# Performance work log

Measured on AMD Instinct MI355X. Metric: run time of the kernel, lower is better.

The kernel has to match this reference:

```python
import jax, jax.numpy as jnp
import numpy as np

N_NODES = 50000
N_EDGES = 800000
FEATURES = 64
HIDDEN = 128
OUT_DIM = 64
CUTOFF = 10.0
STEP = 0.1
N_MU = 100  # len(arange(0, 10, 0.1))


def setup_inputs() -> dict:
    key = jax.random.key(0)
    k_h, k_src, k_dst, k_norm, k_w1, k_w2 = jax.random.split(key, 6)
    h = jax.random.normal(k_h, (N_NODES, FEATURES), dtype=jnp.float32)
    src = jax.random.randint(k_src, (N_EDGES,), 0, N_NODES, dtype=jnp.int64)
    dst = jax.random.randint(k_dst, (N_EDGES,), 0, N_NODES, dtype=jnp.int64)
    edge_norm = jax.random.uniform(k_norm, (N_EDGES,), dtype=jnp.float32) * CUTOFF
    mu = jnp.arange(0.0, CUTOFF, STEP, dtype=jnp.float32)  # [100], learned param
    in_dim = 2 * FEATURES + N_MU
    # xavier_normal with gain split across 2 linear layers: layer_gain = 1.0
    s1 = float(np.sqrt(2.0 / (in_dim + HIDDEN)))
    s2 = float(np.sqrt(2.0 / (HIDDEN + OUT_DIM)))
    W1 = jax.random.normal(k_w1, (HIDDEN, in_dim), dtype=jnp.float32) * s1
    W2 = jax.random.normal(k_w2, (OUT_DIM, HIDDEN), dtype=jnp.float32) * s2
    return {"h": h, "src": src, "dst": dst, "edge_norm": edge_norm,
            "mu": mu, "W1": W1, "W2": W2}


def reference(h, src, dst, edge_norm, mu, W1, W2):
    # Gaussian RBF expansion of edge distances: [E, n_mu]
    d_emb = jnp.exp((-1.0 / STEP) * (mu[None, :] - edge_norm[:, None]) ** 2)
    # gather endpoint features and concat: [E, 2*features + n_mu]
    x = jnp.concatenate((h[src], h[dst], d_emb), axis=-1)
    # MLP: Linear(no bias) -> SiLU -> Linear(no bias)
    hdn = jax.nn.silu(x @ W1.T)
    return hdn @ W2.T
```

## Files before the change

kernel.cpp:

```cpp
#include <hip/hip_runtime.h>
#include <hip/hip_bf16.h>

#define FEAT     64
#define NMU      100
#define K1_REAL  228
#define K1_PAD   256
#define HID      128
#define ODIM     64
#define K2       128
#define MTILE    64
#define LDA1     264
#define LDH      132

typedef __bf16 bf16x8 __attribute__((ext_vector_type(8)));
typedef __bf16 bf16x4 __attribute__((ext_vector_type(4)));
typedef float  fx4    __attribute__((ext_vector_type(4)));

__global__ void pack_w(const float* __restrict__ W1, const float* __restrict__ W2,
                       __bf16* __restrict__ B1, __bf16* __restrict__ B2) {
    int i = blockIdx.x * 256 + threadIdx.x;
    if (i < 32768) {
        int j  = i & 7;
        int n  = (i >> 3) & 127;
        int qk = i >> 10;
        int k  = (qk >> 2) * 32 + (qk & 3) * 8 + j;
        float v = (k < K1_REAL) ? W1[n * K1_REAL + k] : 0.0f;
        B1[i] = (__bf16)v;
    } else {
        int t = i - 32768;
        int j  = t & 7;
        int n  = (t >> 3) & 63;
        int qk = t >> 9;
        int k  = (qk >> 2) * 32 + (qk & 3) * 8 + j;
        B2[t] = (__bf16)W2[n * K2 + k];
    }
}

__global__ __launch_bounds__(256)
void edges_fused(const float* __restrict__ h,
                 const int*   __restrict__ src,
                 const int*   __restrict__ dst,
                 const float* __restrict__ enorm,
                 const float* __restrict__ mu,
                 const __bf16* __restrict__ B1,
                 const __bf16* __restrict__ B2,
                 float* __restrict__ out) {
    __shared__ __bf16 S[MTILE * LDA1];
    __bf16* Atile = S;
    __bf16* Htile = S;

    const int tid = threadIdx.x;
    const int e0  = blockIdx.x * MTILE;

    {
        int r = tid >> 2, p = tid & 3;
        int e = e0 + r;
        int node = (p < 2) ? src[e] : dst[e];
        int half = p & 1;
        const float4* hp = (const float4*)(h + (size_t)node * FEAT + half * 32);
        __bf16* ap = &Atile[r * LDA1 + (p >> 1) * FEAT + half * 32];
#pragma unroll
        for (int i = 0; i < 8; ++i) {
            float4 v = hp[i];
            bf16x4 o = { (__bf16)v.x, (__bf16)v.y, (__bf16)v.z, (__bf16)v.w };
            *(bf16x4*)(ap + i * 4) = o;
        }
    }
    {
        int r = tid >> 2, g = tid & 3;
        float d = enorm[e0 + r];
        __bf16* ap = &Atile[r * LDA1 + 2 * FEAT];
        int j0 = g * 25;
#pragma unroll
        for (int jj = 0; jj < 25; ++jj) {
            int j = j0 + jj;
            float t = mu[j] - d;
            ap[j] = (__bf16)__expf(-10.0f * t * t);
        }
        __bf16* zp = &Atile[r * LDA1 + K1_REAL + g * 7];
#pragma unroll
        for (int c = 0; c < 7; ++c) zp[c] = (__bf16)0.0f;
    }
    __syncthreads();

    const int lane = tid & 63;
    const int w    = tid >> 6;
    const int ln   = lane & 15;
    const int q    = lane >> 4;

    fx4 acc[4][2];
#pragma unroll
    for (int mt = 0; mt < 4; ++mt)
#pragma unroll
        for (int ntl = 0; ntl < 2; ++ntl)
            acc[mt][ntl] = (fx4){0.f, 0.f, 0.f, 0.f};

    const bf16x8* pB1 = (const bf16x8*)B1;
#pragma unroll
    for (int kk = 0; kk < 8; ++kk) {
        const int kof = kk * 32 + q * 8;
        bf16x8 a[4];
#pragma unroll
        for (int mt = 0; mt < 4; ++mt)
            a[mt] = *(const bf16x8*)&Atile[(mt * 16 + ln) * LDA1 + kof];
        bf16x8 b[2];
#pragma unroll
        for (int ntl = 0; ntl < 2; ++ntl)
            b[ntl] = pB1[(kk * 4 + q) * 128 + (w * 2 + ntl) * 16 + ln];
#pragma unroll
        for (int mt = 0; mt < 4; ++mt)
#pragma unroll
            for (int ntl = 0; ntl < 2; ++ntl)
                acc[mt][ntl] = __builtin_amdgcn_mfma_f32_16x16x32_bf16(
                    a[mt], b[ntl], acc[mt][ntl], 0, 0, 0);
    }

    __syncthreads();

#pragma unroll
    for (int mt = 0; mt < 4; ++mt) {
#pragma unroll
        for (int ntl = 0; ntl < 2; ++ntl) {
#pragma unroll
            for (int r = 0; r < 4; ++r) {
                float z = acc[mt][ntl][r];
                float s = z / (1.0f + __expf(-z));
                int row = mt * 16 + q * 4 + r;
                int col = (w * 2 + ntl) * 16 + ln;
                Htile[row * LDH + col] = (__bf16)s;
            }
        }
    }
    __syncthreads();

    fx4 acc2[4];
#pragma unroll
    for (int mt = 0; mt < 4; ++mt) acc2[mt] = (fx4){0.f, 0.f, 0.f, 0.f};

    const bf16x8* pB2 = (const bf16x8*)B2;
#pragma unroll
    for (int kk = 0; kk < 4; ++kk) {
        const int kof = kk * 32 + q * 8;
        bf16x8 b2 = pB2[(kk * 4 + q) * 64 + w * 16 + ln];
#pragma unroll
        for (int mt = 0; mt < 4; ++mt) {
            bf16x8 a2 = *(const bf16x8*)&Htile[(mt * 16 + ln) * LDH + kof];
            acc2[mt] = __builtin_amdgcn_mfma_f32_16x16x32_bf16(a2, b2, acc2[mt], 0, 0, 0);
        }
    }

#pragma unroll
    for (int mt = 0; mt < 4; ++mt) {
#pragma unroll
        for (int r = 0; r < 4; ++r) {
            int row = mt * 16 + q * 4 + r;
            int col = w * 16 + ln;
            out[(size_t)(e0 + row) * ODIM + col] = acc2[mt][r];
        }
    }
}

extern "C" void kernel_launch(void* const* d_in, const int* in_sizes, int n_in,
                              void* d_out, int out_size, void* d_ws, size_t ws_size,
                              hipStream_t stream) {
    const float* h   = (const float*)d_in[0];
    const int*   src = (const int*)d_in[1];
    const int*   dst = (const int*)d_in[2];
    const float* en  = (const float*)d_in[3];
    const float* mu  = (const float*)d_in[4];
    const float* W1  = (const float*)d_in[5];
    const float* W2  = (const float*)d_in[6];

    __bf16* B1 = (__bf16*)d_ws;
    __bf16* B2 = (__bf16*)((char*)d_ws + 65536);

    pack_w<<<160, 256, 0, stream>>>(W1, W2, B1, B2);

    const int E = in_sizes[1];
    const int nblocks = E / MTILE;
    edges_fused<<<nblocks, 256, 0, stream>>>(h, src, dst, en, mu, B1, B2, (float*)d_out);
}
```

Measured before the change: 372.2 us.

## Give each wave its own edge tile and build MFMA A-fragments in registers

Each wave now owns 32 edges and computes all 128 hidden columns itself. The A operands (gathered node features and RBF values) are built directly in registers from global memory instead of being staged through a shared-memory tile. This removes the block-wide __syncthreads barriers and the LDS round-trip for the first GEMM. In exchange it uses more accumulator registers (launch bounds of 4 blocks per CU) and each wave reloads the full B1 and B2 weights from global/L2.

```diff
diff --git a/kernel.cpp b/kernel.cpp
--- a/kernel.cpp
+++ b/kernel.cpp
@@ -1,19 +1,18 @@
 #include <hip/hip_runtime.h>
 #include <hip/hip_bf16.h>
+
 
 #define FEAT     64
 #define NMU      100
 #define K1_REAL  228
-#define K1_PAD   256
 #define HID      128
 #define ODIM     64
 #define K2       128
-#define MTILE    64
-#define LDA1     264
-#define LDH      132
+#define WEDGES   32
+#define BEDGES   128
+#define LDH2     136
 
 typedef __bf16 bf16x8 __attribute__((ext_vector_type(8)));
-typedef __bf16 bf16x4 __attribute__((ext_vector_type(4)));
 typedef float  fx4    __attribute__((ext_vector_type(4)));
 
 __global__ void pack_w(const float* __restrict__ W1, const float* __restrict__ W2,
@@ -36,7 +35,16 @@
     }
 }
 
-__global__ __launch_bounds__(256)
+__device__ __forceinline__ bf16x8 hfrag(const float* __restrict__ h, int node, int cb) {
+    const float4* p = (const float4*)(h + (size_t)node * FEAT + cb);
+    float4 v0 = p[0];
+    float4 v1 = p[1];
+    bf16x8 a = { (__bf16)v0.x, (__bf16)v0.y, (__bf16)v0.z, (__bf16)v0.w,
+                 (__bf16)v1.x, (__bf16)v1.y, (__bf16)v1.z, (__bf16)v1.w };
+    return a;
+}
+
+__global__ __launch_bounds__(256, 4)
 void edges_fused(const float* __restrict__ h,
                  const int*   __restrict__ src,
                  const int*   __restrict__ dst,
@@ -45,119 +53,139 @@
                  const __bf16* __restrict__ B1,
                  const __bf16* __restrict__ B2,
                  float* __restrict__ out) {
-    __shared__ __bf16 S[MTILE * LDA1];
-    __bf16* Atile = S;
-    __bf16* Htile = S;
-
-    const int tid = threadIdx.x;
-    const int e0  = blockIdx.x * MTILE;
-
-    {
-        int r = tid >> 2, p = tid & 3;
-        int e = e0 + r;
-        int node = (p < 2) ? src[e] : dst[e];
-        int half = p & 1;
-        const float4* hp = (const float4*)(h + (size_t)node * FEAT + half * 32);
-        __bf16* ap = &Atile[r * LDA1 + (p >> 1) * FEAT + half * 32];
-#pragma unroll
-        for (int i = 0; i < 8; ++i) {
-            float4 v = hp[i];
-            bf16x4 o = { (__bf16)v.x, (__bf16)v.y, (__bf16)v.z, (__bf16)v.w };
-            *(bf16x4*)(ap + i * 4) = o;
-        }
-    }
-    {
-        int r = tid >> 2, g = tid & 3;
-        float d = enorm[e0 + r];
-        __bf16* ap = &Atile[r * LDA1 + 2 * FEAT];
-        int j0 = g * 25;
-#pragma unroll
-        for (int jj = 0; jj < 25; ++jj) {
-            int j = j0 + jj;
-            float t = mu[j] - d;
-            ap[j] = (__bf16)__expf(-10.0f * t * t);
-        }
-        __bf16* zp = &Atile[r * LDA1 + K1_REAL + g * 7];
-#pragma unroll
-        for (int c = 0; c < 7; ++c) zp[c] = (__bf16)0.0f;
-    }
-    __syncthreads();
-
+    __shared__ __bf16 Hs[4 * WEDGES * LDH2];
+
+    const int tid  = threadIdx.x;
+    const int w    = tid >> 6;
     const int lane = tid & 63;
-    const int w    = tid >> 6;
     const int ln   = lane & 15;
     const int q    = lane >> 4;
-
-    fx4 acc[4][2];
-#pragma unroll
-    for (int mt = 0; mt < 4; ++mt)
-#pragma unroll
-        for (int ntl = 0; ntl < 2; ++ntl)
-            acc[mt][ntl] = (fx4){0.f, 0.f, 0.f, 0.f};
+    const int g0   = blockIdx.x * BEDGES + w * WEDGES;
+
+    int nsrc[2], ndst[2];
+    float dval[2];
+#pragma unroll
+    for (int mt = 0; mt < 2; ++mt) {
+        int e = g0 + mt * 16 + ln;
+        nsrc[mt] = src[e];
+        ndst[mt] = dst[e];
+        dval[mt] = enorm[e];
+    }
+
+    fx4 acc1[2][8];
+#pragma unroll
+    for (int mt = 0; mt < 2; ++mt)
+#pragma unroll
+        for (int nt = 0; nt < 8; ++nt)
+            acc1[mt][nt] = (fx4){0.f, 0.f, 0.f, 0.f};
 
     const bf16x8* pB1 = (const bf16x8*)B1;
-#pragma unroll
-    for (int kk = 0; kk < 8; ++kk) {
-        const int kof = kk * 32 + q * 8;
-        bf16x8 a[4];
-#pragma unroll
-        for (int mt = 0; mt < 4; ++mt)
-            a[mt] = *(const bf16x8*)&Atile[(mt * 16 + ln) * LDA1 + kof];
-        bf16x8 b[2];
-#pragma unroll
-        for (int ntl = 0; ntl < 2; ++ntl)
-            b[ntl] = pB1[(kk * 4 + q) * 128 + (w * 2 + ntl) * 16 + ln];
-#pragma unroll
-        for (int mt = 0; mt < 4; ++mt)
-#pragma unroll
-            for (int ntl = 0; ntl < 2; ++ntl)
-                acc[mt][ntl] = __builtin_amdgcn_mfma_f32_16x16x32_bf16(
-                    a[mt], b[ntl], acc[mt][ntl], 0, 0, 0);
-    }
-
-    __syncthreads();
-
-#pragma unroll
-    for (int mt = 0; mt < 4; ++mt) {
-#pragma unroll
-        for (int ntl = 0; ntl < 2; ++ntl) {
+
+#pragma unroll
+    for (int kk = 0; kk < 4; ++kk) {
+        const int cb = (kk & 1) * 32 + q * 8;
+        bf16x8 a[2];
+#pragma unroll
+        for (int mt = 0; mt < 2; ++mt) {
+            int node = (kk < 2) ? nsrc[mt] : ndst[mt];
+            a[mt] = hfrag(h, node, cb);
+        }
+#pragma unroll
+        for (int nt = 0; nt < 8; ++nt) {
+            bf16x8 b = pB1[(kk * 4 + q) * 128 + nt * 16 + ln];
+            acc1[0][nt] = __builtin_amdgcn_mfma_f32_16x16x32_bf16(a[0], b, acc1[0][nt], 0, 0, 0);
+            acc1[1][nt] = __builtin_amdgcn_mfma_f32_16x16x32_bf16(a[1], b, acc1[1][nt], 0, 0, 0);
+        }
+    }
+
+#pragma unroll
+    for (int kk = 4; kk < 7; ++kk) {
+        const int c0 = (kk - 4) * 32 + q * 8;
+        float4 m0 = *(const float4*)(mu + c0);
+        float4 m1 = *(const float4*)(mu + c0 + 4);
+        bf16x8 a[2];
+#pragma unroll
+        for (int mt = 0; mt < 2; ++mt) {
+            float d = dval[mt];
+            float t0 = m0.x - d, t1 = m0.y - d, t2 = m0.z - d, t3 = m0.w - d;
+            float t4 = m1.x - d, t5 = m1.y - d, t6 = m1.z - d, t7 = m1.w - d;
+            a[mt] = (bf16x8){ (__bf16)__expf(-10.f * t0 * t0), (__bf16)__expf(-10.f * t1 * t1),
+                              (__bf16)__expf(-10.f * t2 * t2), (__bf16)__expf(-10.f * t3 * t3),
+                              (__bf16)__expf(-10.f * t4 * t4), (__bf16)__expf(-10.f * t5 * t5),
+                              (__bf16)__expf(-10.f * t6 * t6), (__bf16)__expf(-10.f * t7 * t7) };
+        }
+#pragma unroll
+        for (int nt = 0; nt < 8; ++nt) {
+            bf16x8 b = pB1[(kk * 4 + q) * 128 + nt * 16 + ln];
+            acc1[0][nt] = __builtin_amdgcn_mfma_f32_16x16x32_bf16(a[0], b, acc1[0][nt], 0, 0, 0);
+            acc1[1][nt] = __builtin_amdgcn_mfma_f32_16x16x32_bf16(a[1], b, acc1[1][nt], 0, 0, 0);
+        }
+    }
+
+    {
+        float4 m7 = *(const float4*)(mu + 96);
+        const __bf16 zz = (__bf16)0.0f;
+        const bool qz = (q == 0);
+        bf16x8 a[2];
+#pragma unroll
+        for (int mt = 0; mt < 2; ++mt) {
+            float d = dval[mt];
+            float t0 = m7.x - d, t1 = m7.y - d, t2 = m7.z - d, t3 = m7.w - d;
+            a[mt] = (bf16x8){ qz ? (__bf16)__expf(-10.f * t0 * t0) : zz,
+                              qz ? (__bf16)__expf(-10.f * t1 * t1) : zz,
+                              qz ? (__bf16)__expf(-10.f * t2 * t2) : zz,
+                              qz ? (__bf16)__expf(-10.f * t3 * t3) : zz,
+                              zz, zz, zz, zz };
+        }
+#pragma unroll
+        for (int nt = 0; nt < 8; ++nt) {
+            bf16x8 b = pB1[(7 * 4 + q) * 128 + nt * 16 + ln];
+            acc1[0][nt] = __builtin_amdgcn_mfma_f32_16x16x32_bf16(a[0], b, acc1[0][nt], 0, 0, 0);
+            acc1[1][nt] = __builtin_amdgcn_mfma_f32_16x16x32_bf16(a[1], b, acc1[1][nt], 0, 0, 0);
+        }
+    }
+
+    __bf16* Hw = &Hs[w * WEDGES * LDH2];
+#pragma unroll
+    for (int mt = 0; mt < 2; ++mt)
+#pragma unroll
+        for (int nt = 0; nt < 8; ++nt)
 #pragma unroll
             for (int r = 0; r < 4; ++r) {
-                float z = acc[mt][ntl][r];
+                float z = acc1[mt][nt][r];
                 float s = z / (1.0f + __expf(-z));
-                int row = mt * 16 + q * 4 + r;
-                int col = (w * 2 + ntl) * 16 + ln;
-                Htile[row * LDH + col] = (__bf16)s;
+                Hw[(mt * 16 + q * 4 + r) * LDH2 + nt * 16 + ln] = (__bf16)s;
             }
-        }
-    }
-    __syncthreads();
-
-    fx4 acc2[4];
-#pragma unroll
-    for (int mt = 0; mt < 4; ++mt) acc2[mt] = (fx4){0.f, 0.f, 0.f, 0.f};
+
+    fx4 acc2[2][4];
+#pragma unroll
+    for (int mt = 0; mt < 2; ++mt)
+#pragma unroll
+        for (int nt = 0; nt < 4; ++nt)
+            acc2[mt][nt] = (fx4){0.f, 0.f, 0.f, 0.f};
 
     const bf16x8* pB2 = (const bf16x8*)B2;
 #pragma unroll
     for (int kk = 0; kk < 4; ++kk) {
-        const int kof = kk * 32 + q * 8;
-        bf16x8 b2 = pB2[(kk * 4 + q) * 64 + w * 16 + ln];
-#pragma unroll
-        for (int mt = 0; mt < 4; ++mt) {
-            bf16x8 a2 = *(const bf16x8*)&Htile[(mt * 16 + ln) * LDH + kof];
-            acc2[mt] = __builtin_amdgcn_mfma_f32_16x16x32_bf16(a2, b2, acc2[mt], 0, 0, 0);
-        }
-    }
-
-#pragma unroll
-    for (int mt = 0; mt < 4; ++mt) {
-#pragma unroll
-        for (int r = 0; r < 4; ++r) {
-            int row = mt * 16 + q * 4 + r;
-            int col = w * 16 + ln;
-            out[(size_t)(e0 + row) * ODIM + col] = acc2[mt][r];
-        }
-    }
+        bf16x8 a2[2];
+#pragma unroll
+        for (int mt = 0; mt < 2; ++mt)
+            a2[mt] = *(const bf16x8*)&Hw[(mt * 16 + ln) * LDH2 + kk * 32 + q * 8];
+#pragma unroll
+        for (int nt = 0; nt < 4; ++nt) {
+            bf16x8 b2 = pB2[(kk * 4 + q) * 64 + nt * 16 + ln];
+            acc2[0][nt] = __builtin_amdgcn_mfma_f32_16x16x32_bf16(a2[0], b2, acc2[0][nt], 0, 0, 0);
+            acc2[1][nt] = __builtin_amdgcn_mfma_f32_16x16x32_bf16(a2[1], b2, acc2[1][nt], 0, 0, 0);
+        }
+    }
+
+#pragma unroll
+    for (int mt = 0; mt < 2; ++mt)
+#pragma unroll
+        for (int nt = 0; nt < 4; ++nt)
+#pragma unroll
+            for (int r = 0; r < 4; ++r)
+                out[(size_t)(g0 + mt * 16 + q * 4 + r) * ODIM + nt * 16 + ln] = acc2[mt][nt][r];
 }
 
 extern "C" void kernel_launch(void* const* d_in, const int* in_sizes, int n_in,
@@ -177,6 +205,6 @@
     pack_w<<<160, 256, 0, stream>>>(W1, W2, B1, B2);
 
     const int E = in_sizes[1];
-    const int nblocks = E / MTILE;
+    const int nblocks = E / BEDGES;
     edges_fused<<<nblocks, 256, 0, stream>>>(h, src, dst, en, mu, B1, B2, (float*)d_out);
 }
```

After: 338.2 us. 9.1% less time.
